# Kernel optimization log

Measured on AMD Instinct MI355X. Metric: run time of the kernel, lower is better.

The kernel has to match this reference:

```python
import jax, jax.numpy as jnp
import numpy as np

EMB = 1024
HEAD = 64
RANK = 8
LRA_SCL = 2.0
LORA = 1.0


def setup_inputs() -> dict:
    key = jax.random.key(0)
    ks = jax.random.split(key, 12)
    s = 1.0 / np.sqrt(EMB)
    sr = 1.0 / np.sqrt(RANK)
    inp = {
        "batEmb": jax.random.normal(ks[0], (8, 2048, EMB), dtype=jnp.float32),
        "tokMrk": jax.random.randint(ks[1], (8, 2048), 0, 2, dtype=jnp.int32),
        # base projections, nn.Linear weight layout [out, in]
        "Wq": jax.random.uniform(ks[2], (HEAD, EMB), jnp.float32, -s, s),
        "Wk": jax.random.uniform(ks[3], (HEAD, EMB), jnp.float32, -s, s),
        "Wv": jax.random.uniform(ks[4], (HEAD, EMB), jnp.float32, -s, s),
        # LoRA: A [rank, emb], B [head, rank]. (Original inits B to zero; we
        # randomize with small scale so the LoRA path is numerically exercised.)
        "Aq": jax.random.uniform(ks[5], (RANK, EMB), jnp.float32, -s, s),
        "Bq": jax.random.uniform(ks[6], (HEAD, RANK), jnp.float32, -sr, sr) * 0.02,
        "Ak": jax.random.uniform(ks[7], (RANK, EMB), jnp.float32, -s, s),
        "Bk": jax.random.uniform(ks[8], (HEAD, RANK), jnp.float32, -sr, sr) * 0.02,
        "Av": jax.random.uniform(ks[9], (RANK, EMB), jnp.float32, -s, s),
        "Bv": jax.random.uniform(ks[10], (HEAD, RANK), jnp.float32, -sr, sr) * 0.02,
    }
    return inp


def _proj(x, W, A, B):
    # base + LoRA low-rank delta (dropout = identity in eval)
    base = jnp.einsum('bse,he->bsh', x, W)
    lora = jnp.einsum('bsr,hr->bsh', jnp.einsum('bse,re->bsr', x, A), B)
    return base + lora * (LRA_SCL * LORA)


def reference(batEmb, tokMrk, Wq, Wk, Wv, Aq, Bq, Ak, Bk, Av, Bv):
    q = _proj(batEmb, Wq, Aq, Bq)  # [B,S,H]
    k = _proj(batEmb, Wk, Ak, Bk)
    v = _proj(batEmb, Wv, Av, Bv)
    w = jnp.einsum('bqh,bkh->bqk', q, k) * (HEAD ** -0.5)  # [B,S,S]
    mask = (tokMrk == 0)[:, None, :]  # [B,1,S] over key dim
    w = jnp.where(mask, -jnp.inf, w)
    w = jax.nn.softmax(w, axis=-1)
    w = jnp.nan_to_num(w, nan=0.0)
    return jnp.einsum('bqk,bkh->bqh', w, v)
```

## Files before the change

kernel.cpp:

```cpp
#include <hip/hip_runtime.h>
#include <hip/hip_bf16.h>
#include <stdint.h>

#define EMB 1024
#define NB 8
#define SEQ 2048
#define RANK 8
#define SPLIT 4

#define BM 32
#define BK 64
#define NSTG 16
#define XBUF 8192
#define WBUF 24576

typedef __attribute__((ext_vector_type(8))) short bf16x8;
typedef __attribute__((ext_vector_type(4))) float f32x4;
typedef unsigned short u16;
typedef unsigned int u32;

__device__ __forceinline__ u16 f2bf(float f) {
  u32 u = __builtin_bit_cast(u32, f);
  u = (u + 0x7fffu + ((u >> 16) & 1u)) >> 16;
  return (u16)u;
}
__device__ __forceinline__ u32 pk2(float lo, float hi) {
  return (u32)f2bf(lo) | ((u32)f2bf(hi) << 16);
}
__device__ __forceinline__ u32 cvtpk(float lo, float hi) {
  __hip_bfloat162 h = __float22bfloat162_rn(make_float2(lo, hi));
  u32 u; __builtin_memcpy(&u, &h, 4); return u;
}
__device__ __forceinline__ void gll16(const void* g, void* l) {
  __builtin_amdgcn_global_load_lds(
      (const __attribute__((address_space(1))) unsigned int*)g,
      (__attribute__((address_space(3))) unsigned int*)l, 16, 0, 0);
}

#define PBAR()   asm volatile("s_barrier" ::: "memory")
#define WAITV(n) asm volatile("s_waitcnt vmcnt(" #n ")" ::: "memory")

__global__ __launch_bounds__(256) void fold_k(
    const float* __restrict__ Wq, const float* __restrict__ Wk, const float* __restrict__ Wv,
    const float* __restrict__ Aq, const float* __restrict__ Bq,
    const float* __restrict__ Ak, const float* __restrict__ Bk,
    const float* __restrict__ Av, const float* __restrict__ Bv,
    u16* __restrict__ weff) {
  int m = blockIdx.x;
  int mat = m >> 6, h = m & 63;
  const float* W = mat == 0 ? Wq : (mat == 1 ? Wk : Wv);
  const float* A = mat == 0 ? Aq : (mat == 1 ? Ak : Av);
  const float* B = mat == 0 ? Bq : (mat == 1 ? Bk : Bv);
  float bb[RANK];
#pragma unroll
  for (int r = 0; r < RANK; r++) bb[r] = 2.0f * B[h * RANK + r];
  int e = threadIdx.x * 4;
  float4 w4 = *(const float4*)(W + h * EMB + e);
  float a0 = w4.x, a1 = w4.y, a2 = w4.z, a3 = w4.w;
#pragma unroll
  for (int r = 0; r < RANK; r++) {
    float4 av = *(const float4*)(A + r * EMB + e);
    a0 += bb[r] * av.x; a1 += bb[r] * av.y; a2 += bb[r] * av.z; a3 += bb[r] * av.w;
  }
  u16* o = weff + (size_t)m * EMB + e;
  o[0] = f2bf(a0); o[1] = f2bf(a1); o[2] = f2bf(a2); o[3] = f2bf(a3);
}

__global__ __launch_bounds__(320) void proj_k(
    const float* __restrict__ X, const u16* __restrict__ weff,
    u16* __restrict__ qws, u16* __restrict__ kws, u16* __restrict__ vws) {
  extern __shared__ __align__(16) char smem[];
  char* xsm = smem;
  char* wsm = smem + 3 * XBUF;

  int t = threadIdx.x;
  int w = t >> 6, l = t & 63;
  int rbase = blockIdx.x * BM;

  if (w >= 3) {
    int q = w - 3;
    int lr4 = l >> 4;
    int l15 = l & 15;
    int wc0 = l >> 3;
    int wkoff = ((l & 7) ^ wc0) * 8;

#define ISSX(st, bufp) do {                                                    \
    _Pragma("unroll")                                                          \
    for (int i_ = 0; i_ < 2; i_++) {                                           \
      int rrel_ = q * 16 + i_ * 8 + lr4 * 2 + (l15 >> 3);                      \
      int sl_ = l15 & 7;                                 \
      (void)sl_;                                                               \
    } } while (0)
#undef ISSX

#define ISSUE_X(st, bufp) do {                                                 \
    _Pragma("unroll")                                                          \
    for (int i_ = 0; i_ < 4; i_++) {                                           \
      int rrel_ = q * 16 + i_ * 4 + lr4;                                       \
      int xo_ = 4 * (l15 ^ (rrel_ & 7));        \
      gll16(X + (size_t)(rbase + rrel_) * EMB + (st) * BK + xo_,               \
            (bufp) + q * 4096 + i_ * 1024);                                    \
    } } while (0)

#define ISSUE_W(st, bufp) do {                                                 \
    _Pragma("unroll")                                                          \
    for (int i_ = 0; i_ < 12; i_++) { int wj_ = q * 12 + i_;                   \
      gll16(weff + (size_t)(wj_ * 8 + wc0) * EMB + (st) * BK + wkoff,          \
            (bufp) + wj_ * 1024);                                              \
    } } while (0)

    ISSUE_W(0, wsm);
    ISSUE_X(0, xsm);
    ISSUE_X(1, xsm + XBUF);
    WAITV(4);
    PBAR();
    for (int s = 0; s < NSTG; s++) {
      if (s + 1 < NSTG) ISSUE_W(s + 1, wsm + ((s + 1) & 1) * WBUF);
      if (s + 2 < NSTG) ISSUE_X(s + 2, xsm + ((s + 2) % 3) * XBUF);
      if (s + 1 < NSTG) {
        if (s + 2 < NSTG) { WAITV(4); } else { WAITV(0); }
        PBAR();
      }
    }
#undef ISSUE_X
#undef ISSUE_W
  } else {
    int l15 = l & 15, lh = l >> 4;
    f32x4 acc[2][4];
    f32x4 zero = {0.f, 0.f, 0.f, 0.f};
#pragma unroll
    for (int rt = 0; rt < 2; rt++)
#pragma unroll
      for (int ct = 0; ct < 4; ct++) acc[rt][ct] = zero;

    for (int s = 0; s < NSTG; s++) {
      PBAR();
      const char* bx = xsm + (s % 3) * XBUF;
      const char* bw = wsm + (s & 1) * WBUF;
#pragma unroll
      for (int j = 0; j < 2; j++) {
        bf16x8 a[2];
#pragma unroll
        for (int rt = 0; rt < 2; rt++) {
          int r = rt * 16 + l15;
          int sw = (r & 7) << 4;
          const char* base = bx + r * 256;
          f32x4 lo = *(const f32x4*)(base + ((j * 128 + lh * 32) ^ sw));
          f32x4 hi = *(const f32x4*)(base + ((j * 128 + lh * 32 + 16) ^ sw));
          union { bf16x8 v; u32 u[4]; } au;
          au.u[0] = cvtpk(lo.x, lo.y); au.u[1] = cvtpk(lo.z, lo.w);
          au.u[2] = cvtpk(hi.x, hi.y); au.u[3] = cvtpk(hi.z, hi.w);
          a[rt] = au.v;
        }
        __builtin_amdgcn_s_setprio(1);
#pragma unroll
        for (int ct = 0; ct < 4; ct++) {
          int col = w * 64 + ct * 16 + l15;
          bf16x8 bf = *(const bf16x8*)(bw + col * 128 +
                                       ((j * 64 + lh * 16) ^ ((col & 7) << 4)));
#pragma unroll
          for (int rt = 0; rt < 2; rt++)
            acc[rt][ct] = __builtin_amdgcn_mfma_f32_16x16x32_bf16(a[rt], bf, acc[rt][ct], 0, 0, 0);
        }
        __builtin_amdgcn_s_setprio(0);
      }
    }

#pragma unroll
    for (int rt = 0; rt < 2; rt++)
#pragma unroll
      for (int ct = 0; ct < 4; ct++) {
        int c = w * 64 + ct * 16 + l15;
#pragma unroll
        for (int r = 0; r < 4; r++) {
          int rr = rbase + rt * 16 + lh * 4 + r;
          float av = acc[rt][ct][r];
          if (c < 64) av *= 0.125f;
          u16 v = f2bf(av);
          if (c < 64) {
            qws[(size_t)rr * 64 + c] = v;
          } else if (c < 128) {
            kws[(size_t)rr * 64 + (c - 64)] = v;
          } else {
            int bb = rr >> 11, tok = rr & 2047;
            vws[((size_t)(bb * 64 + (c - 128))) * SEQ + tok] = v;
          }
        }
      }
  }
}

__global__ __launch_bounds__(256) void attn_k(
    const u16* __restrict__ qws, const u16* __restrict__ kws, const u16* __restrict__ vws,
    const int* __restrict__ mrk,
    float* __restrict__ po, float* __restrict__ pmp, float* __restrict__ plp) {
  __shared__ __align__(16) u16 ks[2 * 4096];
  __shared__ __align__(16) u16 vt[2 * 4096];
  __shared__ __align__(16) u16 ps[4 * 1024];

  int b = blockIdx.y;
  int z = blockIdx.z;
  int q0 = blockIdx.x * 64;
  int t = threadIdx.x;
  int w = t >> 6, l = t & 63;
  int l15 = l & 15, lh = l >> 4;

  int srow = t >> 3;
  int ssw = (((t & 7) << 4) ^ ((srow & 7) << 4)) >> 1;
  char* ksb = (char*)ks + w * 1024;
  char* vtb = (char*)vt + w * 1024;

  const u16* qp = qws + ((size_t)(b * SEQ + q0 + w * 16 + l15)) * 64 + lh * 8;
  bf16x8 qb0 = *(const bf16x8*)qp;
  bf16x8 qb1 = *(const bf16x8*)(qp + 32);

  f32x4 o[4];
  f32x4 zero = {0.f, 0.f, 0.f, 0.f};
#pragma unroll
  for (int ht = 0; ht < 4; ht++) o[ht] = zero;
  float mrow = -30000.0f, lrow = 0.f;

  int swz = (l15 & 7) << 4;
  int koffA = ((lh << 4) ^ swz) >> 1;
  int koffB = ((64 | (lh << 4)) ^ swz) >> 1;
  u16* psw = ps + w * 1024 + l15 * 64;

  const int NC = SEQ / 64 / SPLIT;
  int kk0 = z * (SEQ / SPLIT);

#define STAGE_KV(buf, kk)                                                          \
  do {                                                                             \
    gll16(kws + ((size_t)(b * SEQ + (kk) + srow)) * 64 + ssw,                      \
          ksb + (buf) * 8192);                                                     \
    gll16(kws + ((size_t)(b * SEQ + (kk) + srow + 32)) * 64 + ssw,                 \
          ksb + (buf) * 8192 + 4096);                                              \
    gll16(vws + ((size_t)(b * 64 + srow)) * SEQ + (kk) + ssw,                      \
          vtb + (buf) * 8192);                                                     \
    gll16(vws + ((size_t)(b * 64 + srow + 32)) * SEQ + (kk) + ssw,                 \
          vtb + (buf) * 8192 + 4096);                                              \
  } while (0)

  STAGE_KV(0, kk0);
  __syncthreads();

  int cur = 0;
  for (int kc = 0; kc < NC; kc++) {
    int kk = kk0 + kc * 64;
    if (kc + 1 < NC) STAGE_KV(cur ^ 1, kk + 64);

    int4 mi[4];
#pragma unroll
    for (int nt = 0; nt < 4; nt++)
      mi[nt] = *(const int4*)(mrk + b * SEQ + kk + nt * 16 + lh * 4);

    const u16* kb = ks + cur * 4096;
    f32x4 sa[4];
    __builtin_amdgcn_s_setprio(1);
#pragma unroll
    for (int nt = 0; nt < 4; nt++) {
      const u16* kr = kb + (nt * 16 + l15) * 64;
      bf16x8 k0 = *(const bf16x8*)(kr + koffA);
      bf16x8 k1 = *(const bf16x8*)(kr + koffB);
      f32x4 s = zero;
      s = __builtin_amdgcn_mfma_f32_16x16x32_bf16(k0, qb0, s, 0, 0, 0);
      s = __builtin_amdgcn_mfma_f32_16x16x32_bf16(k1, qb1, s, 0, 0, 0);
      sa[nt] = s;
    }
    __builtin_amdgcn_s_setprio(0);

    const u16* vbb = vt + cur * 4096;
    bf16x8 vb[4][2];
#pragma unroll
    for (int ht = 0; ht < 4; ht++) {
      const u16* vr = vbb + (ht * 16 + l15) * 64;
      vb[ht][0] = *(const bf16x8*)(vr + koffA);
      vb[ht][1] = *(const bf16x8*)(vr + koffB);
    }

#pragma unroll
    for (int nt = 0; nt < 4; nt++) {
      sa[nt][0] = mi[nt].x ? sa[nt][0] : -INFINITY;
      sa[nt][1] = mi[nt].y ? sa[nt][1] : -INFINITY;
      sa[nt][2] = mi[nt].z ? sa[nt][2] : -INFINITY;
      sa[nt][3] = mi[nt].w ? sa[nt][3] : -INFINITY;
    }
    float t0 = fmaxf(fmaxf(sa[0][0], sa[0][1]), fmaxf(sa[0][2], sa[0][3]));
    float t1 = fmaxf(fmaxf(sa[1][0], sa[1][1]), fmaxf(sa[1][2], sa[1][3]));
    float t2 = fmaxf(fmaxf(sa[2][0], sa[2][1]), fmaxf(sa[2][2], sa[2][3]));
    float t3 = fmaxf(fmaxf(sa[3][0], sa[3][1]), fmaxf(sa[3][2], sa[3][3]));
    float tm = fmaxf(fmaxf(t0, t1), fmaxf(t2, t3));
    tm = fmaxf(tm, __shfl_xor(tm, 16));
    tm = fmaxf(tm, __shfl_xor(tm, 32));

    if (!__all(tm <= mrow + 8.0f)) {
      float nm = fmaxf(mrow, tm);
      float alpha = __expf(mrow - nm);
      mrow = nm;
      lrow *= alpha;
      float a0 = __shfl(alpha, lh * 4 + 0);
      float a1 = __shfl(alpha, lh * 4 + 1);
      float a2 = __shfl(alpha, lh * 4 + 2);
      float a3 = __shfl(alpha, lh * 4 + 3);
#pragma unroll
      for (int ht = 0; ht < 4; ht++) {
        o[ht][0] *= a0; o[ht][1] *= a1; o[ht][2] *= a2; o[ht][3] *= a3;
      }
    }

    float ts = 0.f;
#pragma unroll
    for (int nt = 0; nt < 4; nt++) {
#pragma unroll
      for (int r = 0; r < 4; r++) {
        float p = __expf(sa[nt][r] - mrow);
        sa[nt][r] = p;
        ts += p;
      }
    }
    ts += __shfl_xor(ts, 16);
    ts += __shfl_xor(ts, 32);
    lrow += ts;

#pragma unroll
    for (int nt = 0; nt < 4; nt++) {
      u32 plo = pk2(sa[nt][0], sa[nt][1]);
      u32 phi = pk2(sa[nt][2], sa[nt][3]);
      *(uint2*)&psw[(((nt * 32 + lh * 8) ^ swz) >> 1)] = make_uint2(plo, phi);
    }
    bf16x8 ap0 = *(const bf16x8*)(psw + koffA);
    bf16x8 ap1 = *(const bf16x8*)(psw + koffB);

    __builtin_amdgcn_s_setprio(1);
#pragma unroll
    for (int ht = 0; ht < 4; ht++) {
      o[ht] = __builtin_amdgcn_mfma_f32_16x16x32_bf16(ap0, vb[ht][0], o[ht], 0, 0, 0);
      o[ht] = __builtin_amdgcn_mfma_f32_16x16x32_bf16(ap1, vb[ht][1], o[ht], 0, 0, 0);
    }
    __builtin_amdgcn_s_setprio(0);
    __syncthreads();
    cur ^= 1;
  }
#undef STAGE_KV

#pragma unroll
  for (int r = 0; r < 4; r++) {
    int rr = q0 + w * 16 + lh * 4 + r;
    float* pob = po + ((size_t)z * NB * SEQ + (size_t)b * SEQ + rr) * 64;
#pragma unroll
    for (int ht = 0; ht < 4; ht++) pob[ht * 16 + l15] = o[ht][r];
  }
  if (lh == 0) {
    int rr = q0 + w * 16 + l15;
    pmp[(size_t)z * NB * SEQ + (size_t)b * SEQ + rr] = mrow;
    plp[(size_t)z * NB * SEQ + (size_t)b * SEQ + rr] = lrow;
  }
}

__global__ __launch_bounds__(256) void merge_k(
    const float* __restrict__ po, const float* __restrict__ pmp,
    const float* __restrict__ plp, float* __restrict__ out) {
  int tid = threadIdx.x;
  int row = blockIdx.x * 32 + (tid >> 3);
  int c8 = (tid & 7) * 8;
  const int RT = NB * SEQ;

  float m[SPLIT], lv[SPLIT];
  float M = -INFINITY;
#pragma unroll
  for (int s = 0; s < SPLIT; s++) {
    m[s] = pmp[(size_t)s * RT + row];
    lv[s] = plp[(size_t)s * RT + row];
    M = fmaxf(M, m[s]);
  }
  float o8[8];
#pragma unroll
  for (int j = 0; j < 8; j++) o8[j] = 0.f;
  float L = 0.f;
  if (M != -INFINITY) {
#pragma unroll
    for (int s = 0; s < SPLIT; s++) {
      float ws = __expf(m[s] - M);
      L += ws * lv[s];
      const float* p = po + ((size_t)s * RT + row) * 64 + c8;
#pragma unroll
      for (int j = 0; j < 8; j++) o8[j] += ws * p[j];
    }
  }
  float inv = (L > 0.f) ? 1.0f / L : 0.f;
  float* op = out + (size_t)row * 64 + c8;
#pragma unroll
  for (int j = 0; j < 8; j++) op[j] = o8[j] * inv;
}

extern "C" void kernel_launch(void* const* d_in, const int* in_sizes, int n_in,
                              void* d_out, int out_size, void* d_ws, size_t ws_size,
                              hipStream_t stream) {
  const float* X   = (const float*)d_in[0];
  const int*   mrk = (const int*)d_in[1];
  const float* Wq  = (const float*)d_in[2];
  const float* Wk  = (const float*)d_in[3];
  const float* Wv  = (const float*)d_in[4];
  const float* Aq  = (const float*)d_in[5];
  const float* Bq  = (const float*)d_in[6];
  const float* Ak  = (const float*)d_in[7];
  const float* Bk  = (const float*)d_in[8];
  const float* Av  = (const float*)d_in[9];
  const float* Bv  = (const float*)d_in[10];

  u16* weff = (u16*)d_ws;
  u16* qws  = (u16*)((char*)d_ws + (512 << 10));
  u16* kws  = qws + (size_t)16384 * 64;
  u16* vws  = kws + (size_t)16384 * 64;
  float* po  = (float*)((char*)d_ws + ((size_t)6656 << 10));
  float* pmp = po + (size_t)SPLIT * 16384 * 64;
  float* plp = pmp + (size_t)SPLIT * 16384;

  (void)hipFuncSetAttribute((const void*)proj_k,
                            hipFuncAttributeMaxDynamicSharedMemorySize,
                            3 * XBUF + 2 * WBUF);

  fold_k<<<192, 256, 0, stream>>>(Wq, Wk, Wv, Aq, Bq, Ak, Bk, Av, Bv, weff);
  proj_k<<<512, 320, 3 * XBUF + 2 * WBUF, stream>>>(X, weff, qws, kws, vws);
  attn_k<<<dim3(32, 8, SPLIT), 256, 0, stream>>>(qws, kws, vws, mrk, po, pmp, plp);
  merge_k<<<512, 256, 0, stream>>>(po, pmp, plp, (float*)d_out);
}
```

Baseline: 59.08 us.

## Convert X to bf16 in producer waves, use exp2 softmax and LDS mask

The producer waves now load X through registers, convert it to bf16 and write it swizzled into LDS, instead of streaming fp32 via global_load_lds. This halves the X LDS footprint and removes per-fragment conversion from the MFMA waves. In attention, log2(e) is folded into the Q scale so softmax can use exp2f, with the lazy-rescale threshold widened to match. The key mask is precomputed once per block into LDS as additive 0/-inf values rather than reloaded from global memory for every chunk. In exchange the producer takes on the conversion work and needs register staging plus extra waits.

```diff
diff --git a/kernel.cpp b/kernel.cpp
--- a/kernel.cpp
+++ b/kernel.cpp
@@ -11,8 +11,10 @@
 #define BM 32
 #define BK 64
 #define NSTG 16
-#define XBUF 8192
+#define XBUF 4096
 #define WBUF 24576
+
+#define QSCL 0.180336880f
 
 typedef __attribute__((ext_vector_type(8))) short bf16x8;
 typedef __attribute__((ext_vector_type(4))) float f32x4;
@@ -39,6 +41,8 @@
 
 #define PBAR()   asm volatile("s_barrier" ::: "memory")
 #define WAITV(n) asm volatile("s_waitcnt vmcnt(" #n ")" ::: "memory")
+#define WAITL()  asm volatile("s_waitcnt lgkmcnt(0)" ::: "memory")
+#define MEMBAR() asm volatile("" ::: "memory")
 
 __global__ __launch_bounds__(256) void fold_k(
     const float* __restrict__ Wq, const float* __restrict__ Wk, const float* __restrict__ Wv,
@@ -79,51 +83,76 @@
 
   if (w >= 3) {
     int q = w - 3;
-    int lr4 = l >> 4;
-    int l15 = l & 15;
+    int l8 = l >> 3;
+    int l7 = l & 7;
+    const float* xbase = X + (size_t)(rbase + q * 16 + l8) * EMB + l7 * 8;
+    int wdo0 = (q * 16 + 0 + l8) * 128 + (((u32)(l7 ^ l8)) << 4);
+    int wdo1 = (q * 16 + 8 + l8) * 128 + (((u32)(l7 ^ l8)) << 4);
     int wc0 = l >> 3;
     int wkoff = ((l & 7) ^ wc0) * 8;
 
-#define ISSX(st, bufp) do {                                                    \
-    _Pragma("unroll")                                                          \
-    for (int i_ = 0; i_ < 2; i_++) {                                           \
-      int rrel_ = q * 16 + i_ * 8 + lr4 * 2 + (l15 >> 3);                      \
-      int sl_ = l15 & 7;                                 \
-      (void)sl_;                                                               \
+    float4 xA[4], xB[4];
+
+#define LOADX(st, xr) do {                                                 \
+    _Pragma("unroll")                                                      \
+    for (int i_ = 0; i_ < 2; i_++) {                                       \
+      xr[i_*2]   = *(const float4*)(xbase + (size_t)i_ * 8 * EMB + (st) * BK);      \
+      xr[i_*2+1] = *(const float4*)(xbase + (size_t)i_ * 8 * EMB + (st) * BK + 4);  \
     } } while (0)
-#undef ISSX
-
-#define ISSUE_X(st, bufp) do {                                                 \
-    _Pragma("unroll")                                                          \
-    for (int i_ = 0; i_ < 4; i_++) {                                           \
-      int rrel_ = q * 16 + i_ * 4 + lr4;                                       \
-      int xo_ = 4 * (l15 ^ (rrel_ & 7));        \
-      gll16(X + (size_t)(rbase + rrel_) * EMB + (st) * BK + xo_,               \
-            (bufp) + q * 4096 + i_ * 1024);                                    \
+
+#define WRITEX(bufp, xr) do {                                              \
+    uint4 v0_, v1_;                                                        \
+    v0_.x = cvtpk(xr[0].x, xr[0].y); v0_.y = cvtpk(xr[0].z, xr[0].w);      \
+    v0_.z = cvtpk(xr[1].x, xr[1].y); v0_.w = cvtpk(xr[1].z, xr[1].w);      \
+    v1_.x = cvtpk(xr[2].x, xr[2].y); v1_.y = cvtpk(xr[2].z, xr[2].w);      \
+    v1_.z = cvtpk(xr[3].x, xr[3].y); v1_.w = cvtpk(xr[3].z, xr[3].w);      \
+    *(uint4*)((bufp) + wdo0) = v0_;                                        \
+    *(uint4*)((bufp) + wdo1) = v1_;                                        \
+  } while (0)
+
+#define ISSW(st, bufp) do {                                                \
+    _Pragma("unroll")                                                      \
+    for (int i_ = 0; i_ < 12; i_++) { int wj_ = q * 12 + i_;               \
+      gll16(weff + (size_t)(wj_ * 8 + wc0) * EMB + (st) * BK + wkoff,      \
+            (bufp) + wj_ * 1024);                                          \
     } } while (0)
 
-#define ISSUE_W(st, bufp) do {                                                 \
-    _Pragma("unroll")                                                          \
-    for (int i_ = 0; i_ < 12; i_++) { int wj_ = q * 12 + i_;                   \
-      gll16(weff + (size_t)(wj_ * 8 + wc0) * EMB + (st) * BK + wkoff,          \
-            (bufp) + wj_ * 1024);                                              \
-    } } while (0)
-
-    ISSUE_W(0, wsm);
-    ISSUE_X(0, xsm);
-    ISSUE_X(1, xsm + XBUF);
+    LOADX(0, xA);
+    MEMBAR();
+    ISSW(0, wsm);
+    WAITV(12);
+    WRITEX(xsm, xA);
+    MEMBAR();
+    LOADX(1, xB);
     WAITV(4);
+    WAITL();
     PBAR();
-    for (int s = 0; s < NSTG; s++) {
-      if (s + 1 < NSTG) ISSUE_W(s + 1, wsm + ((s + 1) & 1) * WBUF);
-      if (s + 2 < NSTG) ISSUE_X(s + 2, xsm + ((s + 2) % 3) * XBUF);
-      if (s + 1 < NSTG) {
-        if (s + 2 < NSTG) { WAITV(4); } else { WAITV(0); }
-        PBAR();
-      }
-    }
-#undef ISSUE_X
-#undef ISSUE_W
+
+#define PSTEP(s, WR, LD) do {                                              \
+    WAITV(0);                              \
+    ISSW((s) + 1, wsm + (((s) + 1) & 1) * WBUF);   \
+    MEMBAR();                           \
+    LOADX((s) + 2, LD);                                                    \
+    WRITEX(xsm + (((s) + 1) % 3) * XBUF, WR);                              \
+    WAITV(4);                               \
+    WAITL();                                                               \
+    PBAR();                                                 \
+  } while (0)
+
+    for (int s2 = 0; s2 < 14; s2 += 2) {
+      PSTEP(s2, xB, xA);
+      PSTEP(s2 + 1, xA, xB);
+    }
+#undef PSTEP
+    WAITV(0);
+    WRITEX(xsm + (15 % 3) * XBUF, xB);
+    ISSW(15, wsm + WBUF);
+    WAITV(0);
+    WAITL();
+    PBAR();
+#undef LOADX
+#undef WRITEX
+#undef ISSW
   } else {
     int l15 = l & 15, lh = l >> 4;
     f32x4 acc[2][4];
@@ -143,14 +172,8 @@
 #pragma unroll
         for (int rt = 0; rt < 2; rt++) {
           int r = rt * 16 + l15;
-          int sw = (r & 7) << 4;
-          const char* base = bx + r * 256;
-          f32x4 lo = *(const f32x4*)(base + ((j * 128 + lh * 32) ^ sw));
-          f32x4 hi = *(const f32x4*)(base + ((j * 128 + lh * 32 + 16) ^ sw));
-          union { bf16x8 v; u32 u[4]; } au;
-          au.u[0] = cvtpk(lo.x, lo.y); au.u[1] = cvtpk(lo.z, lo.w);
-          au.u[2] = cvtpk(hi.x, hi.y); au.u[3] = cvtpk(hi.z, hi.w);
-          a[rt] = au.v;
+          a[rt] = *(const bf16x8*)(bx + r * 128 +
+                                   ((j * 64 + lh * 16) ^ ((r & 7) << 4)));
         }
         __builtin_amdgcn_s_setprio(1);
 #pragma unroll
@@ -175,7 +198,7 @@
         for (int r = 0; r < 4; r++) {
           int rr = rbase + rt * 16 + lh * 4 + r;
           float av = acc[rt][ct][r];
-          if (c < 64) av *= 0.125f;
+          if (c < 64) av *= QSCL;
           u16 v = f2bf(av);
           if (c < 64) {
             qws[(size_t)rr * 64 + c] = v;
@@ -197,6 +220,7 @@
   __shared__ __align__(16) u16 ks[2 * 4096];
   __shared__ __align__(16) u16 vt[2 * 4096];
   __shared__ __align__(16) u16 ps[4 * 1024];
+  __shared__ __align__(16) float mska[SEQ / SPLIT];
 
   int b = blockIdx.y;
   int z = blockIdx.z;
@@ -241,17 +265,17 @@
   } while (0)
 
   STAGE_KV(0, kk0);
+  {
+    int2 mi2 = *(const int2*)(mrk + b * SEQ + kk0 + t * 2);
+    mska[t * 2]     = mi2.x ? 0.0f : -INFINITY;
+    mska[t * 2 + 1] = mi2.y ? 0.0f : -INFINITY;
+  }
   __syncthreads();
 
   int cur = 0;
   for (int kc = 0; kc < NC; kc++) {
     int kk = kk0 + kc * 64;
     if (kc + 1 < NC) STAGE_KV(cur ^ 1, kk + 64);
-
-    int4 mi[4];
-#pragma unroll
-    for (int nt = 0; nt < 4; nt++)
-      mi[nt] = *(const int4*)(mrk + b * SEQ + kk + nt * 16 + lh * 4);
 
     const u16* kb = ks + cur * 4096;
     f32x4 sa[4];
@@ -279,10 +303,11 @@
 
 #pragma unroll
     for (int nt = 0; nt < 4; nt++) {
-      sa[nt][0] = mi[nt].x ? sa[nt][0] : -INFINITY;
-      sa[nt][1] = mi[nt].y ? sa[nt][1] : -INFINITY;
-      sa[nt][2] = mi[nt].z ? sa[nt][2] : -INFINITY;
-      sa[nt][3] = mi[nt].w ? sa[nt][3] : -INFINITY;
+      f32x4 km = *(const f32x4*)&mska[kc * 64 + nt * 16 + lh * 4];
+      sa[nt][0] += km[0];
+      sa[nt][1] += km[1];
+      sa[nt][2] += km[2];
+      sa[nt][3] += km[3];
     }
     float t0 = fmaxf(fmaxf(sa[0][0], sa[0][1]), fmaxf(sa[0][2], sa[0][3]));
     float t1 = fmaxf(fmaxf(sa[1][0], sa[1][1]), fmaxf(sa[1][2], sa[1][3]));
@@ -292,9 +317,9 @@
     tm = fmaxf(tm, __shfl_xor(tm, 16));
     tm = fmaxf(tm, __shfl_xor(tm, 32));
 
-    if (!__all(tm <= mrow + 8.0f)) {
+    if (!__all(tm <= mrow + 11.5f)) {
       float nm = fmaxf(mrow, tm);
-      float alpha = __expf(mrow - nm);
+      float alpha = exp2f(mrow - nm);
       mrow = nm;
       lrow *= alpha;
       float a0 = __shfl(alpha, lh * 4 + 0);
@@ -312,7 +337,7 @@
     for (int nt = 0; nt < 4; nt++) {
 #pragma unroll
       for (int r = 0; r < 4; r++) {
-        float p = __expf(sa[nt][r] - mrow);
+        float p = exp2f(sa[nt][r] - mrow);
         sa[nt][r] = p;
         ts += p;
       }
@@ -379,7 +404,7 @@
   if (M != -INFINITY) {
 #pragma unroll
     for (int s = 0; s < SPLIT; s++) {
-      float ws = __expf(m[s] - M);
+      float ws = exp2f(m[s] - M);
       L += ws * lv[s];
       const float* p = po + ((size_t)s * RT + row) * 64 + c8;
 #pragma unroll
```

Result: slower. 64.40 us (+9.0%).
